# Optimization experiments

Hardware: AMD Instinct MI355X
Metric: run time of the kernel (lower is better)

## Reference

```python
import jax, jax.numpy as jnp
import numpy as np

SEQ, BATCH, IN = 512, 64, 1024
H, L = 512, 2


def setup_inputs() -> dict:
    key = jax.random.key(0)
    ks = jax.random.split(key, 5)
    s = 0.02
    return {
        "x": jax.random.normal(ks[0], (SEQ, BATCH, IN), dtype=jnp.float32),
        "W_ih": jax.random.normal(ks[1], (L, 2, 4 * H, IN), dtype=jnp.float32) * s,
        "b_ih": jax.random.normal(ks[2], (L, 2, 4 * H), dtype=jnp.float32) * s,
        "W_hh": jax.random.normal(ks[3], (L, 2, 4 * H, H), dtype=jnp.float32) * s,
        "b_hh": jax.random.normal(ks[4], (L, 2, 4 * H), dtype=jnp.float32) * s,
    }


def _run_direction(xs, Wi, bi, Wh, bh, hidden):
    # Precompute the input projection for all timesteps in one big GEMM.
    pre = jnp.einsum("tbd,gd->tbg", xs, Wi) + bi  # [T, B, 4H]

    def step(carry, p):
        h, c = carry
        gates = p + h @ Wh.T + bh
        i, f, g, o = jnp.split(gates, 4, axis=-1)
        # NOTE: faithful to the source module's (nonstandard) gating:
        #   c_t = c_{t-1} * sigmoid(i) + sigmoid(f) * tanh(g)
        c = c * jax.nn.sigmoid(i) + jax.nn.sigmoid(f) * jnp.tanh(g)
        h = jnp.tanh(c) * jax.nn.sigmoid(o)
        return (h, c), h

    B = xs.shape[1]
    h0 = jnp.zeros((B, hidden), xs.dtype)
    c0 = jnp.zeros((B, hidden), xs.dtype)
    _, hs = jax.lax.scan(step, (h0, c0), pre)
    return hs  # [T, B, H]


def reference(x, W_ih, b_ih, W_hh, b_hh):
    hidden = W_hh.shape[-1]
    num_layers = W_ih.shape[0]
    inp = x  # [T, B, D]
    for l in range(num_layers):
        fwd = _run_direction(inp, W_ih[l, 0], b_ih[l, 0], W_hh[l, 0], b_hh[l, 0], hidden)
        bwd = _run_direction(inp[::-1], W_ih[l, 1], b_ih[l, 1], W_hh[l, 1], b_hh[l, 1], hidden)[::-1]
        inp = jnp.concatenate([fwd, bwd], axis=-1)  # [T, B, 2H]
    return inp
```

## Files before the change

### kernel.cpp

```cpp
#include <hip/hip_runtime.h>

#define TSEQ 512
#define BATCH 64
#define DIN 1024
#define HID 512
#define G4 2048
#define CHK 64

typedef __attribute__((ext_vector_type(8))) short short8;
typedef __attribute__((ext_vector_type(4))) float floatx4;

__device__ __forceinline__ floatx4 mfma16(short8 a, short8 b, floatx4 c) {
  return __builtin_amdgcn_mfma_f32_16x16x32_bf16(a, b, c, 0, 0, 0);
}

__device__ __forceinline__ unsigned short f2bf(float f) {
  unsigned int u = __float_as_uint(f);
  unsigned int r = (u + 0x7fffu + ((u >> 16) & 1u)) >> 16;
  return (unsigned short)r;
}

__device__ __forceinline__ float sigm(float x) { return 1.f / (1.f + __expf(-x)); }
__device__ __forceinline__ float tanh_f(float x) {
  float xx = fminf(fmaxf(x, -15.f), 15.f);
  float e = __expf(2.f * xx);
  return (e - 1.f) / (e + 1.f);
}

__global__ void k_convert_x(const float* __restrict__ x, unsigned short* __restrict__ xbf, int n4) {
  int i = blockIdx.x * 256 + threadIdx.x;
  if (i >= n4) return;
  floatx4 v = reinterpret_cast<const floatx4*>(x)[i];
  union { unsigned short us[4]; unsigned long long ull; } pk;
  pk.us[0] = f2bf(v[0]); pk.us[1] = f2bf(v[1]); pk.us[2] = f2bf(v[2]); pk.us[3] = f2bf(v[3]);
  reinterpret_cast<unsigned long long*>(xbf)[i] = pk.ull;
}

__global__ void k_prep_w(const float* __restrict__ W, unsigned short* __restrict__ Wf, int K) {
  int mt = blockIdx.x, kt = blockIdx.y, ld = blockIdx.z;
  int lane = threadIdx.x;
  int rp = mt * 16 + (lane & 15);
  int row = (rp & 3) * HID + (rp >> 2);
  int k0 = kt * 32 + (lane >> 4) * 8;
  const float* src = W + (size_t)ld * G4 * K + (size_t)row * K + k0;
  unsigned short* dst = Wf + (size_t)ld * G4 * K + (((size_t)mt * (K / 32) + kt) * 64 + lane) * 8;
  for (int j = 0; j < 8; ++j) dst[j] = f2bf(src[j]);
}

__global__ void k_prep_bias(const float* __restrict__ bih, const float* __restrict__ bhh,
                            float* __restrict__ biasf) {
  int i = blockIdx.x * 256 + threadIdx.x;
  int ld = i >> 11;
  int rp = i & 2047;
  int row = (rp & 3) * HID + (rp >> 2);
  biasf[i] = bih[ld * G4 + row] + bhh[ld * G4 + row];
}

__global__ __launch_bounds__(256, 2) void k_proj(
    const unsigned short* __restrict__ xin,
    const unsigned short* __restrict__ Wf,
    const float* __restrict__ biasf,
    float* __restrict__ pre,
    int t0) {
  const int dir = blockIdx.z;
  const int w = threadIdx.x >> 6;
  const int lane = threadIdx.x & 63;
  const int quad = lane >> 4, col = lane & 15;
  const int tloc = blockIdx.y * 4 + w;
  const int tg = dir ? (TSEQ - 1 - (t0 + tloc)) : (t0 + tloc);
  const unsigned short* Wd = Wf + (size_t)dir * G4 * DIN;
  const unsigned short* xrow = xin + (size_t)tg * BATCH * DIN;

  floatx4 acc[8][4];
#pragma unroll
  for (int mi = 0; mi < 8; ++mi)
#pragma unroll
    for (int ni = 0; ni < 4; ++ni) acc[mi][ni] = (floatx4){0.f, 0.f, 0.f, 0.f};

#pragma unroll 4
  for (int kt = 0; kt < 32; ++kt) {
    short8 bfr[4];
#pragma unroll
    for (int ni = 0; ni < 4; ++ni) {
      int b = ni * 16 + col;
      bfr[ni] = *reinterpret_cast<const short8*>(xrow + (size_t)b * DIN + kt * 32 + quad * 8);
    }
#pragma unroll
    for (int mi = 0; mi < 8; ++mi) {
      size_t mt = (size_t)(blockIdx.x * 8 + mi);
      short8 afr = *reinterpret_cast<const short8*>(Wd + ((mt * 32 + kt) * 64 + lane) * 8);
#pragma unroll
      for (int ni = 0; ni < 4; ++ni) acc[mi][ni] = mfma16(afr, bfr[ni], acc[mi][ni]);
    }
  }

#pragma unroll
  for (int mi = 0; mi < 8; ++mi) {
    int gbase = blockIdx.x * 128 + mi * 16 + quad * 4;
#pragma unroll
    for (int r = 0; r < 4; ++r) {
      float bv = biasf[dir * G4 + gbase + r];
      float* prow = pre + (((size_t)dir * CHK + tloc) * G4 + gbase + r) * BATCH;
#pragma unroll
      for (int ni = 0; ni < 4; ++ni) prow[ni * 16 + col] = acc[mi][ni][r] + bv;
    }
  }
}

__global__ __launch_bounds__(256, 4) void k_step(
    const unsigned short* __restrict__ Whhf,
    const float* __restrict__ pre,
    unsigned short* act1bf,
    unsigned short* hT2,
    float* cst,
    float* __restrict__ dout,
    int s, int jloc, int layer) {
  const int dir = blockIdx.y;
  const int gb = blockIdx.x;
  const int w = threadIdx.x >> 6;
  const int lane = threadIdx.x & 63;
  const int quad = lane >> 4, col = lane & 15;
  const int b = w * 16 + col;
  const int t = dir ? (TSEQ - 1 - s) : s;

  floatx4 acc[2];
#pragma unroll
  for (int mi = 0; mi < 2; ++mi) {
#pragma unroll
    for (int r = 0; r < 4; ++r) {
      int gp = gb * 32 + mi * 16 + quad * 4 + r;
      acc[mi][r] = pre[(((size_t)dir * CHK + jloc) * G4 + gp) * BATCH + b];
    }
  }

  if (s > 0) {
    const unsigned short* hprev;
    int hstride;
    if (layer == 0) {
      int tp = dir ? t + 1 : t - 1;
      hprev = act1bf + (size_t)tp * BATCH * DIN + dir * HID;
      hstride = DIN;
    } else {
      hprev = hT2 + (size_t)(((s - 1) & 1) * 2 + dir) * BATCH * HID;
      hstride = HID;
    }
    const unsigned short* Wd = Whhf + (size_t)dir * G4 * HID;
#pragma unroll
    for (int kt = 0; kt < 16; ++kt) {
      short8 bfr = *reinterpret_cast<const short8*>(hprev + (size_t)b * hstride + kt * 32 + quad * 8);
#pragma unroll
      for (int mi = 0; mi < 2; ++mi) {
        size_t mt = (size_t)(gb * 2 + mi);
        short8 afr = *reinterpret_cast<const short8*>(Wd + ((mt * 16 + kt) * 64 + lane) * 8);
        acc[mi] = mfma16(afr, bfr, acc[mi]);
      }
    }
  }

  float* cl = cst + ((size_t)layer * 2 + dir) * HID * BATCH;
#pragma unroll
  for (int mi = 0; mi < 2; ++mi) {
    int u = gb * 8 + mi * 4 + quad;
    float si = sigm(acc[mi][0]);
    float sf = sigm(acc[mi][1]);
    float tg = tanh_f(acc[mi][2]);
    float so = sigm(acc[mi][3]);
    float cprev = (s > 0) ? cl[u * BATCH + b] : 0.f;
    float c = cprev * si + sf * tg;
    float h = tanh_f(c) * so;
    cl[u * BATCH + b] = c;
    if (layer == 0) {
      act1bf[((size_t)t * BATCH + b) * DIN + dir * HID + u] = f2bf(h);
    } else {
      hT2[((size_t)((s & 1) * 2 + dir) * BATCH + b) * HID + u] = f2bf(h);
      dout[((size_t)t * BATCH + b) * DIN + dir * HID + u] = h;
    }
  }
}

extern "C" void kernel_launch(void* const* d_in, const int* in_sizes, int n_in,
                              void* d_out, int out_size, void* d_ws, size_t ws_size,
                              hipStream_t stream) {
  const float* x = (const float*)d_in[0];
  const float* W_ih = (const float*)d_in[1];
  const float* b_ih = (const float*)d_in[2];
  const float* W_hh = (const float*)d_in[3];
  const float* b_hh = (const float*)d_in[4];
  float* dout = (float*)d_out;

  char* p = (char*)d_ws;
  auto alloc = [&](size_t bytes) {
    char* r = p;
    p += (bytes + 255) & ~(size_t)255;
    return r;
  };
  unsigned short* xbf    = (unsigned short*)alloc((size_t)TSEQ * BATCH * DIN * 2);
  unsigned short* act1bf = (unsigned short*)alloc((size_t)TSEQ * BATCH * DIN * 2);
  float*          pre    = (float*)alloc((size_t)2 * CHK * G4 * BATCH * 4);
  unsigned short* Wihf   = (unsigned short*)alloc((size_t)4 * G4 * DIN * 2);
  unsigned short* Whhf   = (unsigned short*)alloc((size_t)4 * G4 * HID * 2);
  float*          biasf  = (float*)alloc((size_t)4 * G4 * 4);
  float*          cst    = (float*)alloc((size_t)4 * HID * BATCH * 4);
  unsigned short* hT2    = (unsigned short*)alloc((size_t)4 * BATCH * HID * 2);

  size_t required = (size_t)(p - (char*)d_ws);
  if (ws_size < required) return;

  int n4 = TSEQ * BATCH * DIN / 4;
  k_convert_x<<<dim3((n4 + 255) / 256), dim3(256), 0, stream>>>(x, xbf, n4);
  k_prep_w<<<dim3(G4 / 16, DIN / 32, 4), dim3(64), 0, stream>>>(W_ih, Wihf, DIN);
  k_prep_w<<<dim3(G4 / 16, HID / 32, 4), dim3(64), 0, stream>>>(W_hh, Whhf, HID);
  k_prep_bias<<<dim3(32), dim3(256), 0, stream>>>(b_ih, b_hh, biasf);

  for (int l = 0; l < 2; ++l) {
    const unsigned short* xin = l ? act1bf : xbf;
    const unsigned short* Wfl = Wihf + (size_t)l * 2 * G4 * DIN;
    const unsigned short* Whl = Whhf + (size_t)l * 2 * G4 * HID;
    const float* bfl = biasf + (size_t)l * 2 * G4;
    for (int c = 0; c < TSEQ / CHK; ++c) {
      k_proj<<<dim3(G4 / 128, CHK / 4, 2), dim3(256), 0, stream>>>(xin, Wfl, bfl, pre, c * CHK);
      for (int j = 0; j < CHK; ++j) {
        k_step<<<dim3(G4 / 32, 2), dim3(256), 0, stream>>>(Whl, pre, act1bf, hT2, cst, dout,
                                                           c * CHK + j, j, l);
      }
    }
  }
  (void)in_sizes; (void)n_in; (void)out_size;
}
```

Before: 7.294 ms.

## Replace per-step launches with persistent chunk kernel using grid barrier

Replaces the 64 per-timestep k_step launches per chunk with one persistent k_rec_chunk kernel. It loops over the chunk's steps and synchronises the 64 blocks of each direction through an atomic counter barrier. Recurrent weights and cell state stay in registers across steps instead of being reloaded from global memory each step. The pre layout changes to batch-major so gate pre-activations load and store as float4. This removes launch overhead and repeated weight traffic, but depends on all 128 blocks being co-resident and adds spin-wait cost at every step.

```diff
diff --git a/kernel.cpp b/kernel.cpp
--- a/kernel.cpp
+++ b/kernel.cpp
@@ -97,84 +97,117 @@
 #pragma unroll
   for (int mi = 0; mi < 8; ++mi) {
     int gbase = blockIdx.x * 128 + mi * 16 + quad * 4;
-#pragma unroll
-    for (int r = 0; r < 4; ++r) {
-      float bv = biasf[dir * G4 + gbase + r];
-      float* prow = pre + (((size_t)dir * CHK + tloc) * G4 + gbase + r) * BATCH;
-#pragma unroll
-      for (int ni = 0; ni < 4; ++ni) prow[ni * 16 + col] = acc[mi][ni][r] + bv;
-    }
-  }
-}
-
-__global__ __launch_bounds__(256, 4) void k_step(
+    floatx4 bv = *reinterpret_cast<const floatx4*>(biasf + dir * G4 + gbase);
+#pragma unroll
+    for (int ni = 0; ni < 4; ++ni) {
+      int b = ni * 16 + col;
+      floatx4 v;
+#pragma unroll
+      for (int r = 0; r < 4; ++r) v[r] = acc[mi][ni][r] + bv[r];
+      *reinterpret_cast<floatx4*>(
+          pre + (((size_t)dir * CHK + tloc) * BATCH + b) * G4 + gbase) = v;
+    }
+  }
+}
+
+__global__ __launch_bounds__(256, 1) void k_rec_chunk(
     const unsigned short* __restrict__ Whhf,
     const float* __restrict__ pre,
     unsigned short* act1bf,
     unsigned short* hT2,
     float* cst,
     float* __restrict__ dout,
-    int s, int jloc, int layer) {
+    unsigned int* __restrict__ bar,
+    int s0, int layer, int base_steps) {
   const int dir = blockIdx.y;
   const int gb = blockIdx.x;
+  const int lane = threadIdx.x & 63;
   const int w = threadIdx.x >> 6;
-  const int lane = threadIdx.x & 63;
   const int quad = lane >> 4, col = lane & 15;
   const int b = w * 16 + col;
-  const int t = dir ? (TSEQ - 1 - s) : s;
-
-  floatx4 acc[2];
-#pragma unroll
-  for (int mi = 0; mi < 2; ++mi) {
-#pragma unroll
-    for (int r = 0; r < 4; ++r) {
-      int gp = gb * 32 + mi * 16 + quad * 4 + r;
-      acc[mi][r] = pre[(((size_t)dir * CHK + jloc) * G4 + gp) * BATCH + b];
-    }
-  }
-
-  if (s > 0) {
-    const unsigned short* hprev;
-    int hstride;
-    if (layer == 0) {
-      int tp = dir ? t + 1 : t - 1;
-      hprev = act1bf + (size_t)tp * BATCH * DIN + dir * HID;
-      hstride = DIN;
-    } else {
-      hprev = hT2 + (size_t)(((s - 1) & 1) * 2 + dir) * BATCH * HID;
-      hstride = HID;
-    }
-    const unsigned short* Wd = Whhf + (size_t)dir * G4 * HID;
+
+  const unsigned short* Wd = Whhf + (size_t)dir * G4 * HID;
+  short8 wreg[2][16];
+#pragma unroll
+  for (int mi = 0; mi < 2; ++mi)
 #pragma unroll
     for (int kt = 0; kt < 16; ++kt) {
-      short8 bfr = *reinterpret_cast<const short8*>(hprev + (size_t)b * hstride + kt * 32 + quad * 8);
-#pragma unroll
-      for (int mi = 0; mi < 2; ++mi) {
-        size_t mt = (size_t)(gb * 2 + mi);
-        short8 afr = *reinterpret_cast<const short8*>(Wd + ((mt * 16 + kt) * 64 + lane) * 8);
-        acc[mi] = mfma16(afr, bfr, acc[mi]);
-      }
-    }
-  }
+      size_t mt = (size_t)(gb * 2 + mi);
+      wreg[mi][kt] = *reinterpret_cast<const short8*>(Wd + ((mt * 16 + kt) * 64 + lane) * 8);
+    }
 
   float* cl = cst + ((size_t)layer * 2 + dir) * HID * BATCH;
+  float creg[2];
 #pragma unroll
   for (int mi = 0; mi < 2; ++mi) {
     int u = gb * 8 + mi * 4 + quad;
-    float si = sigm(acc[mi][0]);
-    float sf = sigm(acc[mi][1]);
-    float tg = tanh_f(acc[mi][2]);
-    float so = sigm(acc[mi][3]);
-    float cprev = (s > 0) ? cl[u * BATCH + b] : 0.f;
-    float c = cprev * si + sf * tg;
-    float h = tanh_f(c) * so;
-    cl[u * BATCH + b] = c;
-    if (layer == 0) {
-      act1bf[((size_t)t * BATCH + b) * DIN + dir * HID + u] = f2bf(h);
-    } else {
-      hT2[((size_t)((s & 1) * 2 + dir) * BATCH + b) * HID + u] = f2bf(h);
-      dout[((size_t)t * BATCH + b) * DIN + dir * HID + u] = h;
-    }
+    creg[mi] = (s0 > 0) ? cl[u * BATCH + b] : 0.f;
+  }
+
+  unsigned int* cnt = bar + dir * 64;
+
+  for (int j = 0; j < CHK; ++j) {
+    const int s = s0 + j;
+    const int t = dir ? (TSEQ - 1 - s) : s;
+
+    floatx4 acc[2];
+#pragma unroll
+    for (int mi = 0; mi < 2; ++mi)
+      acc[mi] = *reinterpret_cast<const floatx4*>(
+          pre + (((size_t)dir * CHK + j) * BATCH + b) * G4 + gb * 32 + mi * 16 + quad * 4);
+
+    if (s > 0) {
+      const unsigned short* hprev;
+      int hstride;
+      if (layer == 0) {
+        int tp = dir ? t + 1 : t - 1;
+        hprev = act1bf + (size_t)tp * BATCH * DIN + dir * HID;
+        hstride = DIN;
+      } else {
+        hprev = hT2 + (size_t)(((s - 1) & 1) * 2 + dir) * BATCH * HID;
+        hstride = HID;
+      }
+#pragma unroll
+      for (int kt = 0; kt < 16; ++kt) {
+        short8 bfr = *reinterpret_cast<const short8*>(hprev + (size_t)b * hstride + kt * 32 + quad * 8);
+        acc[0] = mfma16(wreg[0][kt], bfr, acc[0]);
+        acc[1] = mfma16(wreg[1][kt], bfr, acc[1]);
+      }
+    }
+
+#pragma unroll
+    for (int mi = 0; mi < 2; ++mi) {
+      int u = gb * 8 + mi * 4 + quad;
+      float si = sigm(acc[mi][0]);
+      float sf = sigm(acc[mi][1]);
+      float tg = tanh_f(acc[mi][2]);
+      float so = sigm(acc[mi][3]);
+      float c = creg[mi] * si + sf * tg;
+      float h = tanh_f(c) * so;
+      creg[mi] = c;
+      if (layer == 0) {
+        act1bf[((size_t)t * BATCH + b) * DIN + dir * HID + u] = f2bf(h);
+      } else {
+        hT2[((size_t)((s & 1) * 2 + dir) * BATCH + b) * HID + u] = f2bf(h);
+        dout[((size_t)t * BATCH + b) * DIN + dir * HID + u] = h;
+      }
+    }
+
+    __syncthreads();
+    if (threadIdx.x == 0) {
+      __threadfence();
+      __hip_atomic_fetch_add(cnt, 1u, __ATOMIC_RELEASE, __HIP_MEMORY_SCOPE_AGENT);
+      const unsigned int target = (unsigned int)(64 * (base_steps + j + 1));
+      while (__hip_atomic_load(cnt, __ATOMIC_ACQUIRE, __HIP_MEMORY_SCOPE_AGENT) < target) {}
+      __threadfence();
+    }
+    __syncthreads();
+  }
+
+#pragma unroll
+  for (int mi = 0; mi < 2; ++mi) {
+    int u = gb * 8 + mi * 4 + quad;
+    cl[u * BATCH + b] = creg[mi];
   }
 }
 
@@ -202,9 +235,12 @@
   float*          biasf  = (float*)alloc((size_t)4 * G4 * 4);
   float*          cst    = (float*)alloc((size_t)4 * HID * BATCH * 4);
   unsigned short* hT2    = (unsigned short*)alloc((size_t)4 * BATCH * HID * 2);
+  unsigned int*   bar    = (unsigned int*)alloc(512);
 
   size_t required = (size_t)(p - (char*)d_ws);
   if (ws_size < required) return;
+
+  hipMemsetAsync(bar, 0, 512, stream);
 
   int n4 = TSEQ * BATCH * DIN / 4;
   k_convert_x<<<dim3((n4 + 255) / 256), dim3(256), 0, stream>>>(x, xbf, n4);
@@ -219,10 +255,8 @@
     const float* bfl = biasf + (size_t)l * 2 * G4;
     for (int c = 0; c < TSEQ / CHK; ++c) {
       k_proj<<<dim3(G4 / 128, CHK / 4, 2), dim3(256), 0, stream>>>(xin, Wfl, bfl, pre, c * CHK);
-      for (int j = 0; j < CHK; ++j) {
-        k_step<<<dim3(G4 / 32, 2), dim3(256), 0, stream>>>(Whl, pre, act1bf, hT2, cst, dout,
-                                                           c * CHK + j, j, l);
-      }
+      k_rec_chunk<<<dim3(64, 2), dim3(256), 0, stream>>>(
+          Whl, pre, act1bf, hT2, cst, dout, bar, c * CHK, l, (l * 8 + c) * CHK);
     }
   }
   (void)in_sizes; (void)n_in; (void)out_size;
```

Result: slower. 14.89 ms (+104.2%).
